# Optimization experiments

Hardware: AMD Instinct MI355X
Metric: run time of the kernel (lower is better)

## Reference

```python
import jax, jax.numpy as jnp
import numpy as np

NUM_GROUPS = 4   # temporal frames == deformable groups
K = 3            # deformable / fusion kernel size
PAD = 1
MAX_DISP = 7
STRIDE2 = 2


def _conv2d(x, w):
    # 3x3, stride 1, pad 1, no bias, NCHW/OIHW
    return jax.lax.conv_general_dilated(
        x, w, window_strides=(1, 1), padding=((PAD, PAD), (PAD, PAD)),
        dimension_numbers=("NCHW", "OIHW", "NCHW"))


def _correlation(x1, x2):
    """FlowNet/PWC correlation: kernel_size=1, max_displacement=7, stride1=1, stride2=2.
    Output: [B, 49, H, W], mean over channels of shifted dot products."""
    B, C, H, W = x1.shape
    r = MAX_DISP // STRIDE2          # 3 -> 7x7 displacement grid
    m = r * STRIDE2                  # 6 = max shift magnitude
    x2p = jnp.pad(x2, ((0, 0), (0, 0), (m, m), (m, m)))
    outs = []
    for di in range(-r, r + 1):
        for dj in range(-r, r + 1):
            dy, dx = di * STRIDE2, dj * STRIDE2
            sh = x2p[:, :, m + dy:m + dy + H, m + dx:m + dx + W]
            outs.append(jnp.mean(x1 * sh, axis=1))
    return jnp.stack(outs, axis=1)   # [B, 49, H, W]


def _deform_conv(x, offset, weight):
    """Deformable conv v1 (ConvOffset2d): 3x3, stride 1, pad 1, NUM_GROUPS deformable groups.
    offset: [B, G*2*K*K, H, W] laid out as (g, k, {dy,dx})."""
    B, C, H, W = x.shape
    G, K2 = NUM_GROUPS, K * K
    Cg = C // G
    off = offset.reshape(B, G, K2, 2, H, W)
    rel = (jnp.arange(K) - PAD).astype(x.dtype)
    rel_y = jnp.repeat(rel, K).reshape(1, 1, K2, 1, 1)   # kh-major, matches weight flatten
    rel_x = jnp.tile(rel, K).reshape(1, 1, K2, 1, 1)
    iy = jnp.arange(H, dtype=x.dtype).reshape(1, 1, 1, H, 1)
    ix = jnp.arange(W, dtype=x.dtype).reshape(1, 1, 1, 1, W)
    py = iy + rel_y + off[:, :, :, 0]   # [B,G,K2,H,W] sample rows
    px = ix + rel_x + off[:, :, :, 1]   # sample cols
    xg = x.reshape(B, G, Cg, H, W).transpose(0, 1, 3, 4, 2)  # [B,G,H,W,Cg]
    y0 = jnp.floor(py); x0 = jnp.floor(px)
    fy = py - y0; fx = px - x0
    y0 = y0.astype(jnp.int32); x0 = x0.astype(jnp.int32)
    bi = jnp.arange(B).reshape(B, 1, 1, 1, 1)
    gi = jnp.arange(G).reshape(1, G, 1, 1, 1)
    acc = jnp.zeros((B, G, K2, H, W, Cg), x.dtype)
    for dy in (0, 1):
        for dx in (0, 1):
            yy = y0 + dy; xx = x0 + dx
            wgt = (fy if dy else 1.0 - fy) * (fx if dx else 1.0 - fx)
            valid = ((yy >= 0) & (yy < H) & (xx >= 0) & (xx < W)).astype(x.dtype)
            v = xg[bi, gi, jnp.clip(yy, 0, H - 1), jnp.clip(xx, 0, W - 1)]
            acc = acc + v * (wgt * valid)[..., None]
    wr = weight.reshape(weight.shape[0], G, Cg, K2)  # [O,G,Cg,K2]
    return jnp.einsum('bgkhwc,ogck->bohw', acc, wr)


def setup_inputs() -> dict:
    key = jax.random.key(0)
    k0, k1, k2, k3 = jax.random.split(key, 4)
    B, C, H, W = 4, 256, 64, 64
    G = NUM_GROUPS
    inputs = jax.random.normal(k0, (B * G, C, H, W), jnp.float32)
    w_offset = jax.random.normal(k1, (G * 2 * K * K, C + MAX_DISP ** 2, K, K), jnp.float32) * 0.02
    w_def = jax.random.normal(k2, (C, C, K, K), jnp.float32) * 0.02
    w_fusion = jax.random.normal(k3, (C, C * G, K, K), jnp.float32) * 0.02
    return {"inputs": inputs, "w_offset": w_offset, "w_def": w_def,
            "w_fusion": w_fusion, "d1": 0, "d2": 0}


def reference(inputs, w_offset, w_def, w_fusion, d1, d2):
    # d1, d2 are unused by the original forward.
    G = NUM_GROUPS
    y = inputs[G - 1::G]
    _y = jax.lax.stop_gradient(y)
    feats = []
    for ii in range(G - 1):           # n_iter = 1
        x = inputs[ii::G]
        _x = jax.lax.stop_gradient(x)
        corr = _correlation(_x, _y)                       # [B,49,H,W]
        off = _conv2d(jnp.concatenate([x, corr], axis=1), w_offset)
        x = _deform_conv(x, off, w_def)
        feats.append(x)
    return _conv2d(jnp.concatenate(feats + [y], axis=1), w_fusion)
```

## Files before the change

kernel.cpp:

```cpp
#include <hip/hip_runtime.h>

#define HH 64
#define WW 64
#define HW 4096
#define CC 256
#define BB 4
#define GG 4
#define NPAIR 3

typedef __attribute__((ext_vector_type(8))) short short8;
typedef __attribute__((ext_vector_type(4))) float f32x4;
typedef unsigned short ushort_t;

__device__ inline ushort_t f2bf(float x) {
    unsigned int u = __float_as_uint(x);
    unsigned int r = (u + 0x7fffu + ((u >> 16) & 1u)) >> 16;
    return (ushort_t)r;
}
__device__ inline float bflo(unsigned u) { return __uint_as_float(u << 16); }
__device__ inline float bfhi(unsigned u) { return __uint_as_float(u & 0xffff0000u); }

__global__ void prep_all(const float* __restrict__ wd, const float* __restrict__ wo,
                         const float* __restrict__ wf, ushort_t* __restrict__ wdefMF,
                         ushort_t* __restrict__ woffMF, ushort_t* __restrict__ wfusMF) {
    int idx = blockIdx.x * 256 + threadIdx.x;
    if (idx < 589824) {
        int k = idx >> 16;
        int rem = idx & 65535;
        int o = rem >> 8;
        int c = rem & 255;
        wdefMF[idx] = f2bf(wd[((size_t)(o * 256 + c)) * 9 + k]);
        return;
    }
    idx -= 589824;
    if (idx < 230400) {
        int k = idx / (80 * 320);
        int rem = idx % (80 * 320);
        int o = rem / 320;
        int ci = rem % 320;
        woffMF[idx] = (o < 72 && ci < 305) ? f2bf(wo[((size_t)o * 305 + ci) * 9 + k])
                                           : (ushort_t)0;
        return;
    }
    idx -= 230400;
    if (idx < 2359296) {
        int k = idx / (256 * 1024);
        int rem = idx % (256 * 1024);
        int o = rem / 1024;
        int ci = rem % 1024;
        wfusMF[idx] = f2bf(wf[((size_t)o * 1024 + ci) * 9 + k]);
    }
}

__global__ void __launch_bounds__(256) xt_build(const float* __restrict__ in,
                                                ushort_t* __restrict__ XT) {
    __shared__ ushort_t tileT[64][72];
    int hw0 = blockIdx.x * 64;
    int ct = blockIdx.y;
    int z = blockIdx.z;
    int pair = z >> 2, b = z & 3;
    int t = threadIdx.x;
    int cil = t >> 2, q = t & 3;
    const float* sp = in + ((size_t)(b * 4 + pair) * 256 + ct * 64 + cil) * HW + hw0 + q * 16;
#pragma unroll
    for (int i = 0; i < 16; ++i) tileT[q * 16 + i][cil] = f2bf(sp[i]);
    __syncthreads();
    int hwl = t >> 2;
    const uint4* tp = reinterpret_cast<const uint4*>(&tileT[hwl][q * 16]);
    uint4* op = reinterpret_cast<uint4*>(
        &XT[((size_t)z * HW + hw0 + hwl) * 320 + ct * 64 + q * 16]);
    op[0] = tp[0];
    op[1] = tp[1];
}

__global__ void __launch_bounds__(256) ft_build_y(const float* __restrict__ in,
                                                  ushort_t* __restrict__ FT) {
    __shared__ ushort_t tileT[64][72];
    int hw0 = blockIdx.x * 64;
    int ct = blockIdx.y;
    int b = blockIdx.z;
    int t = threadIdx.x;
    int cil = t >> 2, q = t & 3;
    const float* sp = in + ((size_t)(b * 4 + 3) * 256 + ct * 64 + cil) * HW + hw0 + q * 16;
#pragma unroll
    for (int i = 0; i < 16; ++i) tileT[q * 16 + i][cil] = f2bf(sp[i]);
    __syncthreads();
    int hwl = t >> 2;
    const uint4* tp = reinterpret_cast<const uint4*>(&tileT[hwl][q * 16]);
    uint4* op = reinterpret_cast<uint4*>(
        &FT[((size_t)b * HW + hw0 + hwl) * 1024 + 768 + ct * 64 + q * 16]);
    op[0] = tp[0];
    op[1] = tp[1];
}

__global__ void __launch_bounds__(256, 2) corr_mfma(ushort_t* __restrict__ XT,
                                                    const ushort_t* __restrict__ FT) {
    __shared__ ushort_t Al[64][264];
    __shared__ ushort_t Bl[64][264];
    int lin = (blockIdx.x & 7) * 96 + (blockIdx.x >> 3);
    int z = lin >> 6, h = lin & 63;
    int b = z & 3;
    int t = threadIdx.x;
    int ti = t >> 6;
    int l15 = t & 15, kq = (t >> 4) & 3;
    const ushort_t* x1 = XT + ((size_t)z * HW + h * 64) * 320;
    const ushort_t* yb = FT + (size_t)b * HW * 1024 + 768;

    {
        int p = t >> 2, q = t & 3;
        ushort_t* xr = XT + ((size_t)z * HW + h * 64 + p) * 320 + 256 + q * 16;
        uint4 zz = make_uint4(0, 0, 0, 0);
        *reinterpret_cast<uint4*>(xr) = zz;
        *reinterpret_cast<uint4*>(xr + 8) = zz;
    }
    for (int idx = t; idx < 2048; idx += 256) {
        int r = idx >> 5, q = idx & 31;
        *reinterpret_cast<uint4*>(&Al[r][q * 8]) =
            *reinterpret_cast<const uint4*>(x1 + (size_t)r * 320 + q * 8);
    }
    __syncthreads();

    int tj0 = max(ti - 1, 0), tj1 = min(ti + 1, 3);
#pragma unroll 1
    for (int di = 0; di < 7; ++di) {
        int row2 = h + 2 * (di - 3);
        bool vrow = (row2 >= 0) && (row2 < HH);
        if (vrow) {
            for (int idx = t; idx < 2048; idx += 256) {
                int r = idx >> 5, q = idx & 31;
                *reinterpret_cast<uint4*>(&Bl[r][q * 8]) =
                    *reinterpret_cast<const uint4*>(
                        yb + ((size_t)(row2 * 64 + r)) * 1024 + q * 8);
            }
        }
        __syncthreads();
        if (vrow) {
#pragma unroll 1
            for (int tj = tj0; tj <= tj1; ++tj) {
                f32x4 acc = (f32x4){0.f, 0.f, 0.f, 0.f};
#pragma unroll
                for (int cs = 0; cs < 8; ++cs) {
                    int c0 = cs * 32;
                    short8 a = *reinterpret_cast<const short8*>(&Al[ti * 16 + l15][c0 + kq * 8]);
                    short8 bb = *reinterpret_cast<const short8*>(&Bl[tj * 16 + l15][c0 + kq * 8]);
                    acc = __builtin_amdgcn_mfma_f32_16x16x32_bf16(a, bb, acc, 0, 0, 0);
                }
#pragma unroll
                for (int e = 0; e < 4; ++e) {
                    int row = ti * 16 + 4 * kq + e;
                    int col = tj * 16 + l15;
                    int d = col - row + 6;
                    if (d >= 0 && d <= 12 && !(d & 1)) {
                        XT[((size_t)z * HW + h * 64 + row) * 320 + 256 + di * 7 + (d >> 1)] =
                            f2bf(acc[e] * (1.f / 256.f));
                    }
                }
            }
        }
        __syncthreads();
    }
}

__global__ void __launch_bounds__(256, 2) offconv_mfma(const ushort_t* __restrict__ XT,
                                                       const ushort_t* __restrict__ wmf,
                                                       float* __restrict__ off) {
    __shared__ ushort_t a_lds[9][80][40];
    __shared__ ushort_t b_hal[264][40];
    int lin = (blockIdx.x & 7) * 48 + (blockIdx.x >> 3);
    int z = lin >> 5;
    int n0t = lin & 31;
    int h0 = n0t * 2;
    int t = threadIdx.x;
    int wid = t >> 6;
    int lane = t & 63;
    int l15 = lane & 15;
    int kq = lane >> 4;
    const ushort_t* xtb = XT + (size_t)z * HW * 320;

    f32x4 acc[5][2];
#pragma unroll
    for (int m = 0; m < 5; ++m)
#pragma unroll
        for (int n = 0; n < 2; ++n) acc[m][n] = (f32x4){0.f, 0.f, 0.f, 0.f};

#pragma unroll 1
    for (int cs = 0; cs < 10; ++cs) {
        int ci0 = cs * 32;
        __syncthreads();
        for (int idx = t; idx < 264; idx += 256) {
            int r = idx / 66, c = idx - r * 66;
            int hP = h0 + r - 1, wP = c - 1;
            uint4* dst = reinterpret_cast<uint4*>(&b_hal[idx][0]);
            if (hP >= 0 && hP < HH && wP >= 0 && wP < WW) {
                const uint4* src = reinterpret_cast<const uint4*>(
                    xtb + (size_t)(hP * WW + wP) * 320 + ci0);
                dst[0] = src[0];
                dst[1] = src[1];
                dst[2] = src[2];
                dst[3] = src[3];
            } else {
                uint4 zz = make_uint4(0, 0, 0, 0);
                dst[0] = zz;
                dst[1] = zz;
                dst[2] = zz;
                dst[3] = zz;
            }
        }
        for (int idx = t; idx < 2880; idx += 256) {
            int tp = idx / 320;
            int rem = idx - tp * 320;
            int o = rem >> 2, q = rem & 3;
            *reinterpret_cast<uint4*>(&a_lds[tp][o][q * 8]) =
                *reinterpret_cast<const uint4*>(
                    wmf + ((size_t)tp * 80 + o) * 320 + ci0 + q * 8);
        }
        __syncthreads();
#pragma unroll 1
        for (int tap = 0; tap < 9; ++tap) {
            int kh = tap / 3, kw = tap - kh * 3;
            short8 af[5], bf[2];
#pragma unroll
            for (int m = 0; m < 5; ++m)
                af[m] = *reinterpret_cast<const short8*>(&a_lds[tap][m * 16 + l15][kq * 8]);
#pragma unroll
            for (int n = 0; n < 2; ++n) {
                int p = wid * 32 + n * 16 + l15;
                int pos = ((p >> 6) + kh) * 66 + (p & 63) + kw;
                bf[n] = *reinterpret_cast<const short8*>(&b_hal[pos][kq * 8]);
            }
#pragma unroll
            for (int m = 0; m < 5; ++m)
#pragma unroll
                for (int n = 0; n < 2; ++n)
                    acc[m][n] = __builtin_amdgcn_mfma_f32_16x16x32_bf16(af[m], bf[n],
                                                                        acc[m][n], 0, 0, 0);
        }
    }
    float* ob = off + (size_t)z * 72 * HW + h0 * 64 + wid * 32;
#pragma unroll
    for (int m = 0; m < 5; ++m)
#pragma unroll
        for (int n = 0; n < 2; ++n)
#pragma unroll
            for (int e = 0; e < 4; ++e) {
                int o_l = m * 16 + kq * 4 + e;
                if (o_l < 72) ob[(size_t)o_l * HW + n * 16 + l15] = acc[m][n][e];
            }
}

__global__ void __launch_bounds__(256, 3) deform_mfma(const ushort_t* __restrict__ XT,
                                                      const float* __restrict__ off,
                                                      const ushort_t* __restrict__ wmf,
                                                      ushort_t* __restrict__ FT) {
    __shared__ ushort_t b_lds[64][264];
    int u = blockIdx.x & 7, v = blockIdx.x >> 3;
    int lin = u * 96 + v;
    int z = lin >> 6, h = lin & 63;
    int b = z & 3, pair = z >> 2;

    const ushort_t* xtz = XT + (size_t)z * HW * 320;
    const float* offp = off + (size_t)z * 72 * HW;
    int tid = threadIdx.x;
    int lane = tid & 63;
    int g = tid >> 6;
    int l15 = tid & 15;
    int kq = (tid >> 4) & 3;

    f32x4 acc[4][4];
#pragma unroll
    for (int m = 0; m < 4; ++m)
#pragma unroll
        for (int n = 0; n < 4; ++n) acc[m][n] = (f32x4){0.f, 0.f, 0.f, 0.f};

    for (int k = 0; k < 9; ++k) {
        __syncthreads();
        {
            float oy = offp[(size_t)(g * 18 + k * 2 + 0) * HW + h * WW + lane];
            float ox = offp[(size_t)(g * 18 + k * 2 + 1) * HW + h * WW + lane];
            float py = (float)h + (float)(k / 3 - 1) + oy;
            float px = (float)lane + (float)(k % 3 - 1) + ox;
            float y0f = floorf(py), x0f = floorf(px);
            float fy = py - y0f, fx = px - x0f;
            int y0 = (int)y0f, x0 = (int)x0f;
            int y1 = y0 + 1, x1 = x0 + 1;
            bool vy0 = (y0 >= 0) && (y0 < HH);
            bool vy1 = (y1 >= 0) && (y1 < HH);
            bool vx0 = (x0 >= 0) && (x0 < WW);
            bool vx1 = (x1 >= 0) && (x1 < WW);
            float w00 = (1.f - fy) * (1.f - fx) * ((vy0 && vx0) ? 1.f : 0.f);
            float w01 = (1.f - fy) * fx * ((vy0 && vx1) ? 1.f : 0.f);
            float w10 = fy * (1.f - fx) * ((vy1 && vx0) ? 1.f : 0.f);
            float w11 = fy * fx * ((vy1 && vx1) ? 1.f : 0.f);
            int cy0 = min(max(y0, 0), HH - 1), cy1 = min(max(y1, 0), HH - 1);
            int cx0 = min(max(x0, 0), WW - 1), cx1 = min(max(x1, 0), WW - 1);
            const ushort_t* p00 = xtz + (size_t)(cy0 * WW + cx0) * 320 + g * 64;
            const ushort_t* p01 = xtz + (size_t)(cy0 * WW + cx1) * 320 + g * 64;
            const ushort_t* p10 = xtz + (size_t)(cy1 * WW + cx0) * 320 + g * 64;
            const ushort_t* p11 = xtz + (size_t)(cy1 * WW + cx1) * 320 + g * 64;
#pragma unroll
            for (int c0 = 0; c0 < 64; c0 += 8) {
                uint4 a00 = *reinterpret_cast<const uint4*>(p00 + c0);
                uint4 a01 = *reinterpret_cast<const uint4*>(p01 + c0);
                uint4 a10 = *reinterpret_cast<const uint4*>(p10 + c0);
                uint4 a11 = *reinterpret_cast<const uint4*>(p11 + c0);
                unsigned pw[4];
                const unsigned* u00 = &a00.x;
                const unsigned* u01 = &a01.x;
                const unsigned* u10 = &a10.x;
                const unsigned* u11 = &a11.x;
#pragma unroll
                for (int q = 0; q < 4; ++q) {
                    float s0 = w00 * bflo(u00[q]) + w01 * bflo(u01[q]) +
                               w10 * bflo(u10[q]) + w11 * bflo(u11[q]);
                    float s1 = w00 * bfhi(u00[q]) + w01 * bfhi(u01[q]) +
                               w10 * bfhi(u10[q]) + w11 * bfhi(u11[q]);
                    pw[q] = (unsigned)f2bf(s0) | ((unsigned)f2bf(s1) << 16);
                }
                *reinterpret_cast<uint4*>(&b_lds[lane][g * 64 + c0]) =
                    make_uint4(pw[0], pw[1], pw[2], pw[3]);
            }
        }
        __syncthreads();
        const ushort_t* wkbase = wmf + (size_t)k * 65536 + (size_t)(g * 64) * 256;
#pragma unroll 1
        for (int cs = 0; cs < 8; ++cs) {
            int c0 = cs * 32;
            short8 bfr[4], afr[4];
#pragma unroll
            for (int n = 0; n < 4; ++n)
                bfr[n] = *reinterpret_cast<const short8*>(&b_lds[n * 16 + l15][c0 + kq * 8]);
#pragma unroll
            for (int m = 0; m < 4; ++m)
                afr[m] = *reinterpret_cast<const short8*>(
                    wkbase + (size_t)(m * 16 + l15) * 256 + c0 + kq * 8);
#pragma unroll
            for (int m = 0; m < 4; ++m)
#pragma unroll
                for (int n = 0; n < 4; ++n)
                    acc[m][n] = __builtin_amdgcn_mfma_f32_16x16x32_bf16(afr[m], bfr[n],
                                                                        acc[m][n], 0, 0, 0);
        }
    }
    __syncthreads();
#pragma unroll
    for (int m = 0; m < 4; ++m)
#pragma unroll
        for (int n = 0; n < 4; ++n) {
            unsigned lo = (unsigned)f2bf(acc[m][n][0]) | ((unsigned)f2bf(acc[m][n][1]) << 16);
            unsigned hi = (unsigned)f2bf(acc[m][n][2]) | ((unsigned)f2bf(acc[m][n][3]) << 16);
            uint2 vv = make_uint2(lo, hi);
            *reinterpret_cast<uint2*>(&b_lds[n * 16 + l15][g * 64 + m * 16 + kq * 4]) = vv;
        }
    __syncthreads();
    int wout = tid >> 2, ch = tid & 3;
    ushort_t* dst = FT + ((size_t)b * HW + h * 64 + wout) * 1024 + pair * 256 + ch * 64;
    const ushort_t* srcl = &b_lds[wout][ch * 64];
#pragma unroll
    for (int i = 0; i < 8; ++i) {
        uint4 vv = *reinterpret_cast<const uint4*>(srcl + i * 8);
        *reinterpret_cast<uint4*>(dst + i * 8) = vv;
    }
}

__global__ void __launch_bounds__(256, 2) fusion_mfma(const ushort_t* __restrict__ FT,
                                                      const ushort_t* __restrict__ wmf,
                                                      float* __restrict__ out) {
    __shared__ ushort_t a_lds[9][64][40];
    __shared__ ushort_t b_hal[264][40];
    int lin = ((blockIdx.x & 7) << 6) | (blockIdx.x >> 3);
    int ot = lin & 3;
    int g2 = lin >> 2;
    int n0t = g2 & 31;
    int b = g2 >> 5;
    int o0 = ot * 64;
    int h0 = n0t * 2;
    int t = threadIdx.x;
    int wid = t >> 6;
    int lane = t & 63;
    int l15 = lane & 15;
    int kq = lane >> 4;
    const ushort_t* ftb = FT + (size_t)b * HW * 1024;

    f32x4 acc[4][2];
#pragma unroll
    for (int fm = 0; fm < 4; ++fm)
#pragma unroll
        for (int fn = 0; fn < 2; ++fn) acc[fm][fn] = (f32x4){0.f, 0.f, 0.f, 0.f};

#pragma unroll 1
    for (int cs = 0; cs < 32; ++cs) {
        int ci0 = cs * 32;
        __syncthreads();
        for (int idx = t; idx < 264; idx += 256) {
            int r = idx / 66, c = idx - r * 66;
            int hP = h0 + r - 1, wP = c - 1;
            uint4* dst = reinterpret_cast<uint4*>(&b_hal[idx][0]);
            if (hP >= 0 && hP < HH && wP >= 0 && wP < WW) {
                const uint4* src = reinterpret_cast<const uint4*>(
                    ftb + (size_t)(hP * WW + wP) * 1024 + ci0);
                dst[0] = src[0];
                dst[1] = src[1];
                dst[2] = src[2];
                dst[3] = src[3];
            } else {
                uint4 zz = make_uint4(0, 0, 0, 0);
                dst[0] = zz;
                dst[1] = zz;
                dst[2] = zz;
                dst[3] = zz;
            }
        }
        for (int idx = t; idx < 2304; idx += 256) {
            int tp = idx >> 8;
            int rem = idx & 255;
            int o = rem >> 2, q = rem & 3;
            *reinterpret_cast<uint4*>(&a_lds[tp][o][q * 8]) =
                *reinterpret_cast<const uint4*>(
                    wmf + ((size_t)(tp * 256 + o0 + o) << 10) + ci0 + q * 8);
        }
        __syncthreads();
#pragma unroll 1
        for (int tap = 0; tap < 9; ++tap) {
            int kh = tap / 3, kw = tap - kh * 3;
            short8 af[4], bf[2];
#pragma unroll
            for (int m = 0; m < 4; ++m)
                af[m] = *reinterpret_cast<const short8*>(&a_lds[tap][m * 16 + l15][kq * 8]);
#pragma unroll
            for (int n = 0; n < 2; ++n) {
                int p = wid * 32 + n * 16 + l15;
                int pos = ((p >> 6) + kh) * 66 + (p & 63) + kw;
                bf[n] = *reinterpret_cast<const short8*>(&b_hal[pos][kq * 8]);
            }
#pragma unroll
            for (int m = 0; m < 4; ++m)
#pragma unroll
                for (int n = 0; n < 2; ++n)
                    acc[m][n] = __builtin_amdgcn_mfma_f32_16x16x32_bf16(af[m], bf[n],
                                                                        acc[m][n], 0, 0, 0);
        }
    }
    float* ob = out + ((size_t)b * 256 + o0) * HW + h0 * 64 + wid * 32;
#pragma unroll
    for (int fm = 0; fm < 4; ++fm)
#pragma unroll
        for (int fn = 0; fn < 2; ++fn)
#pragma unroll
            for (int e = 0; e < 4; ++e) {
                int o_l = fm * 16 + 4 * kq + e;
                ob[(size_t)o_l * HW + fn * 16 + l15] = acc[fm][fn][e];
            }
}

extern "C" void kernel_launch(void* const* d_in, const int* in_sizes, int n_in,
                              void* d_out, int out_size, void* d_ws, size_t ws_size,
                              hipStream_t stream) {
    const float* in   = (const float*)d_in[0];
    const float* wOff = (const float*)d_in[1];
    const float* wDef = (const float*)d_in[2];
    const float* wFus = (const float*)d_in[3];
    float* out = (float*)d_out;
    char* base = (char*)d_ws;

    ushort_t* XT     = (ushort_t*)base;
    ushort_t* FT     = (ushort_t*)(base + 31457280);
    float* offB      = (float*)(base + 65011712);
    ushort_t* wdefMF = (ushort_t*)(base + 79167488);
    ushort_t* woffMF = (ushort_t*)(base + 80347136);
    ushort_t* wfusMF = (ushort_t*)(base + 80807936);

    hipLaunchKernelGGL(prep_all, dim3((3179520 + 255) / 256), dim3(256), 0, stream,
                       wDef, wOff, wFus, wdefMF, woffMF, wfusMF);
    hipLaunchKernelGGL(xt_build, dim3(64, 4, 12), dim3(256), 0, stream, in, XT);
    hipLaunchKernelGGL(ft_build_y, dim3(64, 4, 4), dim3(256), 0, stream, in, FT);
    hipLaunchKernelGGL(corr_mfma, dim3(768), dim3(256), 0, stream, XT, FT);
    hipLaunchKernelGGL(offconv_mfma, dim3(384), dim3(256), 0, stream, XT, woffMF, offB);
    hipLaunchKernelGGL(deform_mfma, dim3(768), dim3(256), 0, stream, XT, offB, wdefMF, FT);
    hipLaunchKernelGGL(fusion_mfma, dim3(512), dim3(256), 0, stream, FT, wfusMF, out);
}
```

Measured before the change: 473.9 us.

## Register-prefetch next K-slice in fusion conv and merge XT/FT build kernels

The fusion convolution kernel now loads the next channel slice of weights and halo activations into registers while the MFMAs run on the current slice held in LDS. The registers are written to LDS after a barrier, which hides global-load latency behind compute at the cost of about 17 extra uint4 registers per thread and a second barrier per iteration. Separately, the two transpose/convert kernels for x and y are merged into one launch with a z-dimension of 16, removing one kernel launch.

Result: slower. 534.4 us (+12.8%).

```diff
diff --git a/kernel.cpp b/kernel.cpp
--- a/kernel.cpp
+++ b/kernel.cpp
@@ -52,43 +52,37 @@
     }
 }
 
-__global__ void __launch_bounds__(256) xt_build(const float* __restrict__ in,
-                                                ushort_t* __restrict__ XT) {
+__global__ void __launch_bounds__(256) build_xy(const float* __restrict__ in,
+                                                ushort_t* __restrict__ XT,
+                                                ushort_t* __restrict__ FT) {
     __shared__ ushort_t tileT[64][72];
     int hw0 = blockIdx.x * 64;
     int ct = blockIdx.y;
-    int z = blockIdx.z;
-    int pair = z >> 2, b = z & 3;
+    int zz = blockIdx.z;
     int t = threadIdx.x;
     int cil = t >> 2, q = t & 3;
-    const float* sp = in + ((size_t)(b * 4 + pair) * 256 + ct * 64 + cil) * HW + hw0 + q * 16;
+    const float* sp;
+    if (zz < 12) {
+        int pair = zz >> 2, b = zz & 3;
+        sp = in + ((size_t)(b * 4 + pair) * 256 + ct * 64 + cil) * HW + hw0 + q * 16;
+    } else {
+        int b = zz - 12;
+        sp = in + ((size_t)(b * 4 + 3) * 256 + ct * 64 + cil) * HW + hw0 + q * 16;
+    }
 #pragma unroll
     for (int i = 0; i < 16; ++i) tileT[q * 16 + i][cil] = f2bf(sp[i]);
     __syncthreads();
     int hwl = t >> 2;
     const uint4* tp = reinterpret_cast<const uint4*>(&tileT[hwl][q * 16]);
-    uint4* op = reinterpret_cast<uint4*>(
-        &XT[((size_t)z * HW + hw0 + hwl) * 320 + ct * 64 + q * 16]);
-    op[0] = tp[0];
-    op[1] = tp[1];
-}
-
-__global__ void __launch_bounds__(256) ft_build_y(const float* __restrict__ in,
-                                                  ushort_t* __restrict__ FT) {
-    __shared__ ushort_t tileT[64][72];
-    int hw0 = blockIdx.x * 64;
-    int ct = blockIdx.y;
-    int b = blockIdx.z;
-    int t = threadIdx.x;
-    int cil = t >> 2, q = t & 3;
-    const float* sp = in + ((size_t)(b * 4 + 3) * 256 + ct * 64 + cil) * HW + hw0 + q * 16;
-#pragma unroll
-    for (int i = 0; i < 16; ++i) tileT[q * 16 + i][cil] = f2bf(sp[i]);
-    __syncthreads();
-    int hwl = t >> 2;
-    const uint4* tp = reinterpret_cast<const uint4*>(&tileT[hwl][q * 16]);
-    uint4* op = reinterpret_cast<uint4*>(
-        &FT[((size_t)b * HW + hw0 + hwl) * 1024 + 768 + ct * 64 + q * 16]);
+    uint4* op;
+    if (zz < 12) {
+        op = reinterpret_cast<uint4*>(
+            &XT[((size_t)zz * HW + hw0 + hwl) * 320 + ct * 64 + q * 16]);
+    } else {
+        int b = zz - 12;
+        op = reinterpret_cast<uint4*>(
+            &FT[((size_t)b * HW + hw0 + hwl) * 1024 + 768 + ct * 64 + q * 16]);
+    }
     op[0] = tp[0];
     op[1] = tp[1];
 }
@@ -387,38 +381,96 @@
 #pragma unroll
         for (int fn = 0; fn < 2; ++fn) acc[fm][fn] = (f32x4){0.f, 0.f, 0.f, 0.f};
 
-#pragma unroll 1
-    for (int cs = 0; cs < 32; ++cs) {
+    uint4 rA[9];
+    uint4 rB0[4], rB1[4];
+
+    auto loadA = [&](int cs) {
         int ci0 = cs * 32;
-        __syncthreads();
-        for (int idx = t; idx < 264; idx += 256) {
-            int r = idx / 66, c = idx - r * 66;
+#pragma unroll
+        for (int i = 0; i < 9; ++i) {
+            int idx = t + i * 256;
+            int tp = idx >> 8;
+            int rem = idx & 255;
+            int o = rem >> 2, q = rem & 3;
+            rA[i] = *reinterpret_cast<const uint4*>(
+                wmf + ((size_t)(tp * 256 + o0 + o) << 10) + ci0 + q * 8);
+        }
+    };
+    auto loadB = [&](int cs) {
+        int ci0 = cs * 32;
+        {
+            int r = t / 66, c = t - r * 66;
             int hP = h0 + r - 1, wP = c - 1;
-            uint4* dst = reinterpret_cast<uint4*>(&b_hal[idx][0]);
             if (hP >= 0 && hP < HH && wP >= 0 && wP < WW) {
                 const uint4* src = reinterpret_cast<const uint4*>(
                     ftb + (size_t)(hP * WW + wP) * 1024 + ci0);
-                dst[0] = src[0];
-                dst[1] = src[1];
-                dst[2] = src[2];
-                dst[3] = src[3];
+                rB0[0] = src[0];
+                rB0[1] = src[1];
+                rB0[2] = src[2];
+                rB0[3] = src[3];
             } else {
                 uint4 zz = make_uint4(0, 0, 0, 0);
-                dst[0] = zz;
-                dst[1] = zz;
-                dst[2] = zz;
-                dst[3] = zz;
-            }
-        }
-        for (int idx = t; idx < 2304; idx += 256) {
+                rB0[0] = zz;
+                rB0[1] = zz;
+                rB0[2] = zz;
+                rB0[3] = zz;
+            }
+        }
+        if (t < 8) {
+            int idx = 256 + t;
+            int r = idx / 66, c = idx - r * 66;
+            int hP = h0 + r - 1, wP = c - 1;
+            if (hP >= 0 && hP < HH && wP >= 0 && wP < WW) {
+                const uint4* src = reinterpret_cast<const uint4*>(
+                    ftb + (size_t)(hP * WW + wP) * 1024 + ci0);
+                rB1[0] = src[0];
+                rB1[1] = src[1];
+                rB1[2] = src[2];
+                rB1[3] = src[3];
+            } else {
+                uint4 zz = make_uint4(0, 0, 0, 0);
+                rB1[0] = zz;
+                rB1[1] = zz;
+                rB1[2] = zz;
+                rB1[3] = zz;
+            }
+        }
+    };
+    auto writeLDS = [&]() {
+#pragma unroll
+        for (int i = 0; i < 9; ++i) {
+            int idx = t + i * 256;
             int tp = idx >> 8;
             int rem = idx & 255;
             int o = rem >> 2, q = rem & 3;
-            *reinterpret_cast<uint4*>(&a_lds[tp][o][q * 8]) =
-                *reinterpret_cast<const uint4*>(
-                    wmf + ((size_t)(tp * 256 + o0 + o) << 10) + ci0 + q * 8);
-        }
-        __syncthreads();
+            *reinterpret_cast<uint4*>(&a_lds[tp][o][q * 8]) = rA[i];
+        }
+        {
+            uint4* dst = reinterpret_cast<uint4*>(&b_hal[t][0]);
+            dst[0] = rB0[0];
+            dst[1] = rB0[1];
+            dst[2] = rB0[2];
+            dst[3] = rB0[3];
+        }
+        if (t < 8) {
+            uint4* dst = reinterpret_cast<uint4*>(&b_hal[256 + t][0]);
+            dst[0] = rB1[0];
+            dst[1] = rB1[1];
+            dst[2] = rB1[2];
+            dst[3] = rB1[3];
+        }
+    };
+
+    loadA(0);
+    loadB(0);
+#pragma unroll 1
+    for (int cs = 0; cs < 32; ++cs) {
+        writeLDS();
+        __syncthreads();
+        if (cs < 31) {
+            loadA(cs + 1);
+            loadB(cs + 1);
+        }
 #pragma unroll 1
         for (int tap = 0; tap < 9; ++tap) {
             int kh = tap / 3, kw = tap - kh * 3;
@@ -439,6 +491,7 @@
                     acc[m][n] = __builtin_amdgcn_mfma_f32_16x16x32_bf16(af[m], bf[n],
                                                                         acc[m][n], 0, 0, 0);
         }
+        __syncthreads();
     }
     float* ob = out + ((size_t)b * 256 + o0) * HW + h0 * 64 + wid * 32;
 #pragma unroll
@@ -471,8 +524,7 @@
 
     hipLaunchKernelGGL(prep_all, dim3((3179520 + 255) / 256), dim3(256), 0, stream,
                        wDef, wOff, wFus, wdefMF, woffMF, wfusMF);
-    hipLaunchKernelGGL(xt_build, dim3(64, 4, 12), dim3(256), 0, stream, in, XT);
-    hipLaunchKernelGGL(ft_build_y, dim3(64, 4, 4), dim3(256), 0, stream, in, FT);
+    hipLaunchKernelGGL(build_xy, dim3(64, 4, 16), dim3(256), 0, stream, in, XT, FT);
     hipLaunchKernelGGL(corr_mfma, dim3(768), dim3(256), 0, stream, XT, FT);
     hipLaunchKernelGGL(offconv_mfma, dim3(384), dim3(256), 0, stream, XT, woffMF, offB);
     hipLaunchKernelGGL(deform_mfma, dim3(768), dim3(256), 0, stream, XT, offB, wdefMF, FT);
```
